# Kernel tuning notes

Hardware: AMD Instinct MI355X
Metric: run time of the kernel (lower is better)

Reference implementation:

```python
import jax, jax.numpy as jnp
import numpy as np

VOCAB = 1_000_000
TOTAL = 819_200
BATCH = 16_384
DIM = 16


def setup_inputs() -> dict:
    key = jax.random.key(0)
    k1, k2, k3, k4 = jax.random.split(key, 4)
    feature_ids = jax.random.randint(k1, (TOTAL,), 0, VOCAB, dtype=jnp.int64 if jax.config.jax_enable_x64 else jnp.int32)
    feature_ratings = jax.random.uniform(k2, (TOTAL,), dtype=jnp.float32)
    segment_ids = jnp.sort(jax.random.randint(k3, (TOTAL,), 0, BATCH))
    weight = jax.random.normal(k4, (VOCAB, DIM), dtype=jnp.float32)
    bias = jnp.zeros((DIM,), dtype=jnp.float32)
    return {
        "feature_ids": feature_ids,
        "feature_ratings": feature_ratings,
        "segment_ids": segment_ids,
        "batch_size": BATCH,
        "weight": weight,
        "bias": bias,
    }


def reference(feature_ids, feature_ratings, segment_ids, batch_size, weight, bias):
    # gather rows [total, D], weight by per-token rating, ragged segment sum
    rows = weight[feature_ids] * feature_ratings[:, None]
    summed = jax.ops.segment_sum(rows, segment_ids, num_segments=batch_size,
                                 indices_are_sorted=True)
    return summed + bias  # [batch, D]
```

## Files before the change

### kernel.cpp

```cpp
#include <hip/hip_runtime.h>

#define DIM 16

__global__ __launch_bounds__(256) void features_linear_seg_kernel(
    const int*   __restrict__ ids,
    const float* __restrict__ ratings,
    const int*   __restrict__ segs,
    const float* __restrict__ weight,
    const float* __restrict__ bias,
    float*       __restrict__ out,
    int total,
    int batch) {
    int tid = blockIdx.x * blockDim.x + threadIdx.x;
    int d = tid & (DIM - 1);
    int b = tid >> 4;
    if (b >= batch) return;

    int lo0 = 0, n0 = total;
    int lo1 = 0, n1 = total;
    int last = total - 1;
    while ((n0 | n1) != 0) {
        int h0 = n0 >> 1; int m0 = lo0 + h0; m0 = m0 < last ? m0 : last;
        int h1 = n1 >> 1; int m1 = lo1 + h1; m1 = m1 < last ? m1 : last;
        int v0 = segs[m0];
        int v1 = segs[m1];
        bool p0 = (n0 > 0) & (v0 < b);
        bool p1 = (n1 > 0) & (v1 <= b);
        lo0 = p0 ? m0 + 1 : lo0;
        lo1 = p1 ? m1 + 1 : lo1;
        n0  = p0 ? (n0 - h0 - 1) : h0;
        n1  = p1 ? (n1 - h1 - 1) : h1;
    }

    const char* wb = (const char*)weight;
    unsigned db = (unsigned)d << 2;
    float acc = 0.0f;

    int lastt = lo1 - 1;
    for (int base = lo0; base < lo1; base += 16) {
        int   idv[16];
        float rv[16];
        #pragma unroll
        for (int i = 0; i < 16; ++i) {
            int t  = base + i;
            int tc = t < lastt ? t : lastt;
            idv[i] = ids[tc];
            float r = ratings[tc];
            rv[i]  = (t <= lastt) ? r : 0.0f;
        }
        float wv[16];
        #pragma unroll
        for (int i = 0; i < 16; ++i)
            wv[i] = *(const float*)(wb + (((unsigned)idv[i]) << 6) + db);
        #pragma unroll
        for (int i = 0; i < 16; ++i)
            acc = fmaf(wv[i], rv[i], acc);
    }

    out[(((unsigned)b) << 4) + d] = acc + bias[d];
}

extern "C" void kernel_launch(void* const* d_in, const int* in_sizes, int n_in,
                              void* d_out, int out_size, void* d_ws, size_t ws_size,
                              hipStream_t stream) {
    const int*   ids     = (const int*)d_in[0];
    const float* ratings = (const float*)d_in[1];
    const int*   segs    = (const int*)d_in[2];
    const float* weight  = (const float*)d_in[4];
    const float* bias    = (const float*)d_in[5];
    float* out = (float*)d_out;

    int total = in_sizes[0];
    int batch = out_size / DIM;

    long long n_threads = (long long)batch * DIM;
    int threads = 256;
    int blocks = (int)((n_threads + threads - 1) / threads);
    features_linear_seg_kernel<<<blocks, threads, 0, stream>>>(
        ids, ratings, segs, weight, bias, out, total, batch);
}
```

Measured before the change: 119.7 us.

## Switch to token-parallel segment sum with atomic flush and bias-init kernel

Replaces the per-segment binary search over sorted segment ids with a token-parallel scheme. Each block stages 256 tokens in shared memory, and each 16-thread group handles 16 consecutive tokens, accumulating per-dimension and issuing atomicAdds to the output whenever the segment id changes. A separate kernel first initialises the output with the bias. This removes the binary searches and the load imbalance caused by variable segment lengths. In exchange it adds a second launch, float atomics whose summation order is nondeterministic, and contention at segment boundaries.

After: 114.0 us. 1.05x faster.

```diff
diff --git a/kernel.cpp b/kernel.cpp
--- a/kernel.cpp
+++ b/kernel.cpp
@@ -1,63 +1,80 @@
 #include <hip/hip_runtime.h>
 
 #define DIM 16
+#define TOK_PB 256
 
-__global__ __launch_bounds__(256) void features_linear_seg_kernel(
+__global__ void init_out_kernel(float4* __restrict__ out4,
+                                const float* __restrict__ bias,
+                                int n4) {
+    int i = blockIdx.x * blockDim.x + threadIdx.x;
+    if (i < n4) {
+        int d = (i & 3) * 4;
+        out4[i] = make_float4(bias[d], bias[d + 1], bias[d + 2], bias[d + 3]);
+    }
+}
+
+__global__ __launch_bounds__(256, 8) void features_linear_kernel(
     const int*   __restrict__ ids,
     const float* __restrict__ ratings,
     const int*   __restrict__ segs,
     const float* __restrict__ weight,
-    const float* __restrict__ bias,
     float*       __restrict__ out,
-    int total,
-    int batch) {
-    int tid = blockIdx.x * blockDim.x + threadIdx.x;
-    int d = tid & (DIM - 1);
-    int b = tid >> 4;
-    if (b >= batch) return;
+    int total) {
+    __shared__ int   sh_id[TOK_PB];
+    __shared__ float sh_r [TOK_PB];
+    __shared__ int   sh_s [TOK_PB];
 
-    int lo0 = 0, n0 = total;
-    int lo1 = 0, n1 = total;
-    int last = total - 1;
-    while ((n0 | n1) != 0) {
-        int h0 = n0 >> 1; int m0 = lo0 + h0; m0 = m0 < last ? m0 : last;
-        int h1 = n1 >> 1; int m1 = lo1 + h1; m1 = m1 < last ? m1 : last;
-        int v0 = segs[m0];
-        int v1 = segs[m1];
-        bool p0 = (n0 > 0) & (v0 < b);
-        bool p1 = (n1 > 0) & (v1 <= b);
-        lo0 = p0 ? m0 + 1 : lo0;
-        lo1 = p1 ? m1 + 1 : lo1;
-        n0  = p0 ? (n0 - h0 - 1) : h0;
-        n1  = p1 ? (n1 - h1 - 1) : h1;
-    }
+    int j    = threadIdx.x;
+    int t0b  = blockIdx.x * TOK_PB;
+    int nrem = total - t0b;
+    int jc   = j < nrem ? j : nrem - 1;
+    int tj   = t0b + jc;
+    sh_id[j] = ids[tj];
+    sh_r [j] = ratings[tj];
+    sh_s [j] = segs[tj];
+    __syncthreads();
+
+    int d    = j & (DIM - 1);
+    int g    = j >> 4;
+    int base = g << 4;
+    if (base >= nrem) return;
 
     const char* wb = (const char*)weight;
     unsigned db = (unsigned)d << 2;
     float acc = 0.0f;
+    int prev = sh_s[base];
 
-    int lastt = lo1 - 1;
-    for (int base = lo0; base < lo1; base += 16) {
-        int   idv[16];
-        float rv[16];
+    if (base + 16 <= nrem) {
+        int idv[16];
+        #pragma unroll
+        for (int i = 0; i < 16; ++i) idv[i] = sh_id[base + i];
+        float w[16];
+        #pragma unroll
+        for (int i = 0; i < 16; ++i)
+            w[i] = *(const float*)(wb + (((unsigned)idv[i]) << 6) + db);
+
         #pragma unroll
         for (int i = 0; i < 16; ++i) {
-            int t  = base + i;
-            int tc = t < lastt ? t : lastt;
-            idv[i] = ids[tc];
-            float r = ratings[tc];
-            rv[i]  = (t <= lastt) ? r : 0.0f;
+            int   seg = sh_s[base + i];
+            float r   = sh_r[base + i];
+            if (seg != prev) {
+                atomicAdd(&out[prev * DIM + d], acc);
+                acc = 0.0f; prev = seg;
+            }
+            acc = fmaf(w[i], r, acc);
         }
-        float wv[16];
-        #pragma unroll
-        for (int i = 0; i < 16; ++i)
-            wv[i] = *(const float*)(wb + (((unsigned)idv[i]) << 6) + db);
-        #pragma unroll
-        for (int i = 0; i < 16; ++i)
-            acc = fmaf(wv[i], rv[i], acc);
+    } else {
+        for (int i = base; i < nrem; ++i) {
+            int seg = sh_s[i];
+            if (seg != prev) {
+                atomicAdd(&out[prev * DIM + d], acc);
+                acc = 0.0f; prev = seg;
+            }
+            float w = *(const float*)(wb + (((unsigned)sh_id[i]) << 6) + db);
+            acc = fmaf(w, sh_r[i], acc);
+        }
     }
-
-    out[(((unsigned)b) << 4) + d] = acc + bias[d];
+    atomicAdd(&out[prev * DIM + d], acc);
 }
 
 extern "C" void kernel_launch(void* const* d_in, const int* in_sizes, int n_in,
@@ -71,11 +88,17 @@
     float* out = (float*)d_out;
 
     int total = in_sizes[0];
-    int batch = out_size / DIM;
 
-    long long n_threads = (long long)batch * DIM;
-    int threads = 256;
-    int blocks = (int)((n_threads + threads - 1) / threads);
-    features_linear_seg_kernel<<<blocks, threads, 0, stream>>>(
-        ids, ratings, segs, weight, bias, out, total, batch);
+    {
+        int n4 = out_size / 4;
+        int threads = 256;
+        int blocks = (n4 + threads - 1) / threads;
+        init_out_kernel<<<blocks, threads, 0, stream>>>((float4*)out, bias, n4);
+    }
+
+    {
+        int blocks = (total + TOK_PB - 1) / TOK_PB;
+        features_linear_kernel<<<blocks, TOK_PB, 0, stream>>>(
+            ids, ratings, segs, weight, out, total);
+    }
 }
```
